# Performance work log

Measured on AMD Instinct MI355X. Metric: run time of the kernel, lower is better.

Reference implementation:

```python
import jax, jax.numpy as jnp
import numpy as np
from functools import partial

B, S, H = 4, 2048, 1152
NH, HD = 12, 96          # heads, head_dim
NM, MD = 4, 128          # memory heads (indices 6..9), mem_dim
K = 4                    # base kernel
STRIDE = 64              # NeuralMemory chunk stride
INNER = 4 * H            # GLU inner dim
CS_DIL = (1, 2, 4, 8, 16, 32)  # DilatedConvStack: config.dilations[:6]
HEAD_DIL = ((1, 2, 4), (1, 1, 1), (4, 8, 16), (8, 16, 32), (32, 64, 128),
            (64, 128, 256), (256, 512, 1024), (1, 100, 200), (1, 500, 1000),
            (1, 1024, 2048), (3, 9, 27), (5, 25, 125))
MEM_HEADS = (6, 7, 8, 9)


def setup_inputs() -> dict:
    key = jax.random.key(0)
    ks = iter(jax.random.split(key, 48))
    def nrm(shape, s=0.02):
        return jax.random.normal(next(ks), shape, jnp.float32) * s
    return {
        'x': jax.random.normal(next(ks), (B, S, H), jnp.float32),
        'norm1_w': jnp.ones((H,), jnp.float32),
        'norm2_w': jnp.ones((H,), jnp.float32),
        'norm3_w': jnp.ones((H,), jnp.float32),
        'cs_w': nrm((6, H, K), 0.1), 'cs_b': jnp.zeros((6, H), jnp.float32),
        'cs_proj_w': nrm((H, H)), 'cs_proj_b': jnp.zeros((H,), jnp.float32),
        'gate_proj_w': nrm((H, 2 * H)),
        'router_w': nrm((H, NH)), 'router_b': jnp.zeros((NH,), jnp.float32),
        'head_w': nrm((NH, 3, HD, K), 0.1), 'head_b': jnp.zeros((NH, 3, HD), jnp.float32),
        'mem_q': nrm((NM, HD, HD), 0.01), 'mem_k': nrm((NM, HD, HD), 0.01),
        'mem_v': nrm((NM, HD, MD), 0.01), 'mem_gw': nrm((NM, HD)),
        'mem_gb': jnp.full((NM,), -2.0, jnp.float32), 'mem_out': nrm((NM, MD, HD), 0.01),
        'mixgate_w': nrm((H, H)), 'mixgate_b': jnp.full((H,), 2.0, jnp.float32),
        'mixing_w': nrm((H, H)), 'mixing_b': jnp.zeros((H,), jnp.float32),
        'ffn_in_w': nrm((H, 2 * INNER)), 'ffn_out_w': nrm((INNER, H)),
        'cg_w': nrm((H,)), 'cg_b': jnp.float32(1.0),
        'sg_w': nrm((H,)), 'sg_b': jnp.float32(1.0),
        'fg_w': nrm((H,)), 'fg_b': jnp.float32(1.0),
    }


def rmsnorm(x, w, eps=1e-6):
    n = jax.lax.rsqrt(jnp.mean(x * x, axis=-1, keepdims=True) + eps)
    return x * n * w


def dconv(x, w, b, d):
    """Depthwise causal dilated conv. x:[B,S,C], w:[C,K], b:[C]."""
    s = x.shape[1]
    pad = (w.shape[1] - 1) * d
    xp = jnp.pad(x, ((0, 0), (pad, 0), (0, 0)))
    acc = b
    for j in range(w.shape[1]):
        acc = acc + w[:, j] * jax.lax.dynamic_slice_in_dim(xp, j * d, s, axis=1)
    return acc


def conv_stack(x, cs_w, cs_b, proj_w, proj_b):
    h = x
    for i, d in enumerate(CS_DIL):
        h = h + jax.nn.gelu(dconv(h, cs_w[i], cs_b[i], d), approximate=False)
    return h @ proj_w + proj_b


def neural_memory(xm, Wq, Wk, Wv, gw, gb, Wout):
    """Chunked fast-weight memory for NM heads at once. xm:[B,S,NM,HD]."""
    q = jnp.einsum('bsnd,nde->bsne', xm, Wq)
    k = jnp.einsum('bsnd,nde->bsne', xm, Wk)
    v = jnp.einsum('bsnd,ndm->bsnm', xm, Wv)
    g = jax.nn.sigmoid(jnp.einsum('bsnd,nd->bsn', xm, gw) + gb)[..., None]  # [B,S,NM,1]
    nC = S // STRIDE
    def chunk(a):  # [B,S,...] -> [nC,B,STRIDE,...]
        return a.reshape(B, nC, STRIDE, *a.shape[2:]).swapaxes(0, 1)
    q_c, kg_c, v_c = chunk(q), chunk(k * g), chunk(v)
    ga_c = chunk(g).mean(axis=2)[..., None]  # [nC,B,NM,1,1]
    M0 = jnp.zeros((B, NM, HD, MD), xm.dtype)
    def step(M, xs):
        qc, kc, vc, ga = xs
        reads = jnp.einsum('bsnd,bndm->bsnm', qc, M)
        write = jnp.einsum('bsnd,bsnm->bndm', kc, vc)
        return (1.0 - ga) * M + write, reads
    _, reads = jax.lax.scan(step, M0, (q_c, kg_c, v_c, ga_c))
    reads = reads.swapaxes(0, 1).reshape(B, S, NM, MD)
    return jnp.einsum('bsnm,nmd->bsnd', reads, Wout)


def multi_head_state(x, gate_proj_w, router_w, router_b, head_w, head_b,
                     mem_q, mem_k, mem_v, mem_gw, mem_gb, mem_out,
                     mixgate_w, mixgate_b, mixing_w, mixing_b):
    head_weights = jax.nn.sigmoid(x @ router_w + router_b)  # [B,S,NH]
    gp = x @ gate_proj_w
    xg = gp[..., :H] * jax.nn.sigmoid(gp[..., H:])
    xh = xg.reshape(B, S, NH, HD)
    outs = []
    for i in range(NH):
        h = xh[:, :, i, :]
        for j, d in enumerate(HEAD_DIL[i]):
            h = h + dconv(h, head_w[i, j], head_b[i, j], d)
        outs.append(h)
    mem = neural_memory(xh[:, :, MEM_HEADS[0]:MEM_HEADS[-1] + 1, :],
                        mem_q, mem_k, mem_v, mem_gw, mem_gb, mem_out)
    for n, i in enumerate(MEM_HEADS):
        outs[i] = outs[i] + mem[:, :, n, :]
    out = jnp.stack(outs, axis=2) * head_weights[..., None]
    out = out.reshape(B, S, H)
    out = out * jax.nn.sigmoid(out @ mixgate_w + mixgate_b)
    return out @ mixing_w + mixing_b


def glu(x, win, wout):
    h = x @ win
    return (h[..., :INNER] * jax.nn.sigmoid(h[..., INNER:])) @ wout


def reference(x, norm1_w, norm2_w, norm3_w, cs_w, cs_b, cs_proj_w, cs_proj_b,
              gate_proj_w, router_w, router_b, head_w, head_b,
              mem_q, mem_k, mem_v, mem_gw, mem_gb, mem_out,
              mixgate_w, mixgate_b, mixing_w, mixing_b,
              ffn_in_w, ffn_out_w, cg_w, cg_b, sg_w, sg_b, fg_w, fg_b):
    gc = jax.nn.sigmoid(x @ cg_w + cg_b)[..., None]
    x = x + gc * conv_stack(rmsnorm(x, norm1_w), cs_w, cs_b, cs_proj_w, cs_proj_b)
    gs = jax.nn.sigmoid(x @ sg_w + sg_b)[..., None]
    x = x + gs * multi_head_state(rmsnorm(x, norm2_w), gate_proj_w, router_w, router_b,
                                  head_w, head_b, mem_q, mem_k, mem_v, mem_gw, mem_gb,
                                  mem_out, mixgate_w, mixgate_b, mixing_w, mixing_b)
    gf = jax.nn.sigmoid(x @ fg_w + fg_b)[..., None]
    x = x + gf * glu(rmsnorm(x, norm3_w), ffn_in_w, ffn_out_w)
    return x
```

## Files before the change

### kernel.cpp

```cpp
#include <hip/hip_runtime.h>
#include <hip/hip_bf16.h>
#include <math.h>

#define TOKENS 8192
#define HDIM 1152
#define SEQ 2048
#define NHEADS 12
#define HEADD 96
#define NMEM 4
#define MEMD 128
#define FINNER 4608

typedef __hip_bfloat16 bf16;
typedef __attribute__((ext_vector_type(8))) short short8;
typedef __attribute__((ext_vector_type(4))) float floatx4;

__device__ __constant__ int g_hd_dil[NHEADS * 3] = {
    1, 2, 4,   1, 1, 1,    4, 8, 16,   8, 16, 32,
    32, 64, 128, 64, 128, 256, 256, 512, 1024, 1, 100, 200,
    1, 500, 1000, 1, 1024, 2048, 3, 9, 27, 5, 25, 125};

__device__ inline float sigm(float x) { return 1.0f / (1.0f + expf(-x)); }
__device__ inline float gelu_exact(float x) {
  return 0.5f * x * (1.0f + erff(x * 0.70710678118654752f));
}
__device__ inline float wred(float v) {
#pragma unroll
  for (int o = 32; o > 0; o >>= 1) v += __shfl_down(v, o);
  return v;
}
__device__ inline void gl_lds16(const bf16* g, bf16* l) {
  __builtin_amdgcn_global_load_lds(
      (const __attribute__((address_space(1))) unsigned int*)g,
      (__attribute__((address_space(3))) unsigned int*)l, 16, 0, 0);
}

__global__ __launch_bounds__(256) void k_transpose_bf16(
    const float* __restrict__ W, bf16* __restrict__ WT, int K, int N) {
  __shared__ float t[32][33];
  int k0 = blockIdx.y * 32, n0 = blockIdx.x * 32;
  int tx = threadIdx.x & 31, ty = threadIdx.x >> 5;
#pragma unroll
  for (int i = 0; i < 32; i += 8)
    t[ty + i][tx] = W[(size_t)(k0 + ty + i) * N + (n0 + tx)];
  __syncthreads();
#pragma unroll
  for (int i = 0; i < 32; i += 8)
    WT[(size_t)(n0 + ty + i) * K + (k0 + tx)] = __float2bfloat16(t[tx][ty + i]);
}

__global__ __launch_bounds__(256) void k_transpose_pair(
    const float* __restrict__ W, bf16* __restrict__ WT, int K, int N) {
  __shared__ float t[32][33];
  int half = N >> 1;
  int k0 = blockIdx.y * 32, n0 = blockIdx.x * 32;
  int tx = threadIdx.x & 31, ty = threadIdx.x >> 5;
  int c = (tx < 16) ? (n0 / 2 + tx) : (half + n0 / 2 + tx - 16);
#pragma unroll
  for (int i = 0; i < 32; i += 8)
    t[ty + i][tx] = W[(size_t)(k0 + ty + i) * N + c];
  __syncthreads();
#pragma unroll
  for (int i = 0; i < 32; i += 8) {
    int r = ty + i;
    int cc = (r >> 1) + (r & 1) * 16;
    WT[(size_t)(n0 + r) * K + (k0 + tx)] = __float2bfloat16(t[tx][cc]);
  }
}

__global__ __launch_bounds__(256) void k_rms_gate(
    const float* __restrict__ x, const float* __restrict__ nw,
    const float* __restrict__ gw, const float* __restrict__ gb,
    bf16* __restrict__ outb, float* outf, float* __restrict__ gout,
    int writef, const float* __restrict__ rw, const float* __restrict__ rb,
    float* __restrict__ hwout) {
  __shared__ float r1[4], r2[4];
  __shared__ float rr[4][NHEADS];
  int tok = blockIdx.x;
  int tid = threadIdx.x;
  const float* row = x + (size_t)tok * HDIM;
  float a[5];
  float s2 = 0.f, gd = 0.f;
  for (int i = tid, k = 0; i < HDIM; i += 256, ++k) {
    float v = row[i];
    a[k] = v;
    s2 += v * v;
    gd += v * gw[i];
  }
  s2 = wred(s2);
  gd = wred(gd);
  int wave = tid >> 6, lane = tid & 63;
  if (lane == 0) {
    r1[wave] = s2;
    r2[wave] = gd;
  }
  __syncthreads();
  s2 = r1[0] + r1[1] + r1[2] + r1[3];
  gd = r2[0] + r2[1] + r2[2] + r2[3];
  float rn = 1.0f / sqrtf(s2 / (float)HDIM + 1e-6f);
  if (tid == 0) gout[tok] = sigm(gd + gb[0]);
  float racc[NHEADS] = {};
  for (int i = tid, k = 0; i < HDIM; i += 256, ++k) {
    float nv = a[k] * rn * nw[i];
    outb[(size_t)tok * HDIM + i] = __float2bfloat16(nv);
    if (writef) outf[(size_t)tok * HDIM + i] = nv;
    if (hwout) {
      const float* rp = &rw[(size_t)i * NHEADS];
#pragma unroll
      for (int o = 0; o < NHEADS; ++o) racc[o] += nv * rp[o];
    }
  }
  if (hwout) {
#pragma unroll
    for (int o = 0; o < NHEADS; ++o) racc[o] = wred(racc[o]);
    if (lane == 0)
#pragma unroll
      for (int o = 0; o < NHEADS; ++o) rr[wave][o] = racc[o];
    __syncthreads();
    if (tid < NHEADS) {
      float s = rr[0][tid] + rr[1][tid] + rr[2][tid] + rr[3][tid];
      hwout[(size_t)tok * NHEADS + tid] = sigm(s + rb[tid]);
    }
  }
}

#define CS_T 256
#define CS_HALO 189
#define CS_ROWS 445
#define CS_J 28
__global__ __launch_bounds__(256) void k_convstack(
    const bf16* __restrict__ hin, bf16* __restrict__ outb,
    const float* __restrict__ cw, const float* __restrict__ cb) {
  __shared__ float cur[CS_ROWS * 16];
  int bx = blockIdx.x;
  int cs = bx % 72;
  int tile = (bx / 72) & 7;
  int b = bx / 576;
  int c0 = cs * 16;
  int S0 = tile * CS_T;
  int tid = threadIdx.x;
  int c = tid & 15, pg = tid >> 4;
  for (int i = tid; i < CS_ROWS * 8; i += 256) {
    int p = i >> 3, cc2 = (i & 7) * 2;
    int sg = S0 - CS_HALO + p;
    if (sg >= 0) {
      unsigned int u = *reinterpret_cast<const unsigned int*>(
          &hin[((size_t)(b * SEQ + sg)) * HDIM + c0 + cc2]);
      cur[p * 16 + cc2] = __uint_as_float(u << 16);
      cur[p * 16 + cc2 + 1] = __uint_as_float(u & 0xffff0000u);
    } else {
      cur[p * 16 + cc2] = 0.f;
      cur[p * 16 + cc2 + 1] = 0.f;
    }
  }
  const int dil[6] = {1, 2, 4, 8, 16, 32};
  const int Nk[6] = {3, 9, 21, 45, 93, 189};
  float nv[CS_J];
#pragma unroll
  for (int k = 0; k < 6; ++k) {
    int d = dil[k];
    float w0 = cw[((size_t)k * HDIM + c0 + c) * 4 + 0];
    float w1 = cw[((size_t)k * HDIM + c0 + c) * 4 + 1];
    float w2 = cw[((size_t)k * HDIM + c0 + c) * 4 + 2];
    float w3 = cw[((size_t)k * HDIM + c0 + c) * 4 + 3];
    float bb = cb[(size_t)k * HDIM + c0 + c];
    __syncthreads();
#pragma unroll
    for (int j = 0; j < CS_J; ++j) {
      int p = pg + 16 * j;
      if (p >= Nk[k] && p < CS_ROWS) {
        int i = p * 16 + c;
        float acc = bb + w0 * cur[i - 3 * d * 16] + w1 * cur[i - 2 * d * 16] +
                    w2 * cur[i - d * 16] + w3 * cur[i];
        int sg = S0 - CS_HALO + p;
        nv[j] = (sg >= 0) ? (cur[i] + gelu_exact(acc)) : 0.f;
      }
    }
    __syncthreads();
#pragma unroll
    for (int j = 0; j < CS_J; ++j) {
      int p = pg + 16 * j;
      if (p >= Nk[k] && p < CS_ROWS) cur[p * 16 + c] = nv[j];
    }
  }
  __syncthreads();
  for (int r = pg; r < CS_T; r += 16) {
    outb[((size_t)(b * SEQ + S0 + r)) * HDIM + c0 + c] =
        __float2bfloat16(cur[(CS_HALO + r) * 16 + c]);
  }
}

__global__ __launch_bounds__(256) void k_headconv(
    const float* __restrict__ hin, float* __restrict__ hout,
    const float* __restrict__ hw_, const float* __restrict__ hb_, int j) {
  size_t idx4 = (size_t)blockIdx.x * 256 + threadIdx.x;
  if (idx4 >= (size_t)TOKENS * HDIM / 4) return;
  size_t idx = idx4 * 4;
  int c = (int)(idx % HDIM);
  int head = c / HEADD, hd = c % HEADD;
  size_t tok = idx / HDIM;
  int s = (int)(tok % SEQ);
  int d = g_hd_dil[head * 3 + j];
  const float4* wv = reinterpret_cast<const float4*>(
      hw_ + ((size_t)(head * 3 + j) * HEADD + hd) * 4);
  float4 w0 = wv[0], w1 = wv[1], w2 = wv[2], w3 = wv[3];
  float4 bb = *reinterpret_cast<const float4*>(
      &hb_[(size_t)(head * 3 + j) * HEADD + hd]);
  float av0 = bb.x, av1 = bb.y, av2 = bb.z, av3 = bb.w;
  float4 base = *reinterpret_cast<const float4*>(&hin[idx]);
#pragma unroll
  for (int jj = 0; jj < 4; ++jj) {
    int back = (3 - jj) * d;
    if (s - back >= 0) {
      float4 t = *reinterpret_cast<const float4*>(&hin[idx - (size_t)back * HDIM]);
      float a0 = (jj == 0) ? w0.x : (jj == 1) ? w0.y : (jj == 2) ? w0.z : w0.w;
      float a1 = (jj == 0) ? w1.x : (jj == 1) ? w1.y : (jj == 2) ? w1.z : w1.w;
      float a2 = (jj == 0) ? w2.x : (jj == 1) ? w2.y : (jj == 2) ? w2.z : w2.w;
      float a3 = (jj == 0) ? w3.x : (jj == 1) ? w3.y : (jj == 2) ? w3.z : w3.w;
      av0 += a0 * t.x;
      av1 += a1 * t.y;
      av2 += a2 * t.z;
      av3 += a3 * t.w;
    }
  }
  float4 o = {base.x + av0, base.y + av1, base.z + av2, base.w + av3};
  *reinterpret_cast<float4*>(&hout[idx]) = o;
}

template <int MODE>
__global__ __launch_bounds__(256) void k_gemm(
    const bf16* __restrict__ A, const bf16* __restrict__ BT,
    const float* __restrict__ bias, const float* __restrict__ gate,
    const float* addin, float* outf, bf16* outb, int M, int N, int K) {
  __shared__ bf16 As[128 * 64];
  __shared__ bf16 Bs[128 * 64];
  const int tid = threadIdx.x;
  const int m0 = blockIdx.y * 128, n0 = blockIdx.x * 128;
  const int wave = tid >> 6, lane = tid & 63;
  const int wm = (wave & 1) * 64, wn = (wave >> 1) * 64;
  const int l16 = lane & 15, kq = lane >> 4;
  const int srow = lane >> 3;
  const int schunk = ((lane & 7) - srow) & 7;
  const bf16* gA = A + (size_t)(m0 + wave * 32 + srow) * K + schunk * 8;
  const bf16* gB = BT + (size_t)(n0 + wave * 32 + srow) * K + schunk * 8;
  bf16* lA = &As[wave * 32 * 64];
  bf16* lB = &Bs[wave * 32 * 64];
  const size_t rstride = (size_t)8 * K;
  const int col0 = ((kq + l16) & 7) * 8;
  const int col1 = ((kq + 4 + l16) & 7) * 8;
  floatx4 acc[4][4];
  floatx4 zero = {0.f, 0.f, 0.f, 0.f};
#pragma unroll
  for (int i = 0; i < 4; ++i)
#pragma unroll
    for (int jj = 0; jj < 4; ++jj) acc[i][jj] = zero;

  for (int k0 = 0; k0 < K; k0 += 64) {
    __syncthreads();
#pragma unroll
    for (int i = 0; i < 4; ++i) {
      gl_lds16(gA + k0 + i * rstride, lA + i * 8 * 64);
      gl_lds16(gB + k0 + i * rstride, lB + i * 8 * 64);
    }
    __syncthreads();
#pragma unroll
    for (int ks = 0; ks < 2; ++ks) {
      const int col = ks ? col1 : col0;
      short8 af[4], bfr[4];
#pragma unroll
      for (int t = 0; t < 4; ++t) {
        af[t] = *reinterpret_cast<const short8*>(&As[(wm + t * 16 + l16) * 64 + col]);
        bfr[t] = *reinterpret_cast<const short8*>(&Bs[(wn + t * 16 + l16) * 64 + col]);
      }
#pragma unroll
      for (int mt = 0; mt < 4; ++mt)
#pragma unroll
        for (int nt = 0; nt < 4; ++nt)
          acc[mt][nt] = __builtin_amdgcn_mfma_f32_16x16x32_bf16(
              af[mt], bfr[nt], acc[mt][nt], 0, 0, 0);
    }
  }

  if (MODE == 4 || MODE == 5) {
    const int halfN = N >> 1;
#pragma unroll
    for (int mt = 0; mt < 4; ++mt) {
#pragma unroll
      for (int nt = 0; nt < 4; ++nt) {
        int nn = n0 + wn + nt * 16 + l16;
#pragma unroll
        for (int r = 0; r < 4; ++r) {
          float v = acc[mt][nt][r];
          float g = __shfl_xor(v, 1);
          if ((lane & 1) == 0) {
            int m = m0 + wm + mt * 16 + kq * 4 + r;
            float res = v * sigm(g);
            size_t o = (size_t)m * halfN + (nn >> 1);
            if (MODE == 4) outf[o] = res;
            else outb[o] = __float2bfloat16(res);
          }
        }
      }
    }
    return;
  }

#pragma unroll
  for (int mt = 0; mt < 4; ++mt) {
#pragma unroll
    for (int nt = 0; nt < 4; ++nt) {
      int n = n0 + wn + nt * 16 + l16;
      float bv = bias ? bias[n] : 0.f;
#pragma unroll
      for (int r = 0; r < 4; ++r) {
        int m = m0 + wm + mt * 16 + kq * 4 + r;
        float v = acc[mt][nt][r] + bv;
        size_t o = (size_t)m * N + n;
        if (MODE == 2) outf[o] = addin[o] + gate[m] * v;
        else if (MODE == 6) outb[o] = __float2bfloat16(addin[o] * sigm(v));
      }
    }
  }
}

__global__ __launch_bounds__(256) void k_qkvg(
    const float* __restrict__ xh, const float* __restrict__ Wq,
    const float* __restrict__ Wk, const float* __restrict__ Wv,
    const float* __restrict__ gw, const float* __restrict__ gb,
    float* __restrict__ q, float* __restrict__ kg, float* __restrict__ v,
    float* __restrict__ gout) {
  __shared__ float xm[NMEM * HEADD];
  __shared__ float gsh[NMEM];
  int tok = blockIdx.x, tid = threadIdx.x;
  for (int i = tid; i < NMEM * HEADD; i += 256)
    xm[i] = xh[(size_t)tok * HDIM + 6 * HEADD + i];
  __syncthreads();
  if (tid < NMEM) {
    float a = gb[tid];
    for (int d = 0; d < HEADD; ++d) a += xm[tid * HEADD + d] * gw[tid * HEADD + d];
    float s = sigm(a);
    gsh[tid] = s;
    gout[tok * NMEM + tid] = s;
  }
  __syncthreads();
  for (int i = tid; i < 1280; i += 256) {
    if (i < 384) {
      int n = i / HEADD, e = i % HEADD;
      const float* W = Wq + (size_t)n * HEADD * HEADD + e;
      const float* xr = xm + n * HEADD;
      float a = 0.f;
      for (int d = 0; d < HEADD; ++d) a += xr[d] * W[(size_t)d * HEADD];
      q[(size_t)tok * 384 + i] = a;
    } else if (i < 768) {
      int i2 = i - 384;
      int n = i2 / HEADD, e = i2 % HEADD;
      const float* W = Wk + (size_t)n * HEADD * HEADD + e;
      const float* xr = xm + n * HEADD;
      float a = 0.f;
      for (int d = 0; d < HEADD; ++d) a += xr[d] * W[(size_t)d * HEADD];
      kg[(size_t)tok * 384 + i2] = a * gsh[n];
    } else {
      int i2 = i - 768;
      int n = i2 / MEMD, e = i2 % MEMD;
      const float* W = Wv + (size_t)n * HEADD * MEMD + e;
      const float* xr = xm + n * HEADD;
      float a = 0.f;
      for (int d = 0; d < HEADD; ++d) a += xr[d] * W[(size_t)d * MEMD];
      v[(size_t)tok * 512 + i2] = a;
    }
  }
}

__global__ __launch_bounds__(256) void k_memW(const float* __restrict__ kg,
                                              const float* __restrict__ v,
                                              float* __restrict__ W) {
  __shared__ float X[64 * 96];
  __shared__ float V[64 * 128];
  int bx = blockIdx.x;
  int bn = bx >> 5, ch = bx & 31;
  int b = bn >> 2, n = bn & 3;
  int t0 = b * SEQ + ch * 64;
  int tid = threadIdx.x;
  for (int i = tid; i < 64 * 96; i += 256) {
    int s = i / 96, d = i % 96;
    X[i] = kg[((size_t)(t0 + s) * NMEM + n) * HEADD + d];
  }
  for (int i = tid; i < 64 * 128; i += 256) {
    int s = i >> 7, m = i & 127;
    V[i] = v[((size_t)(t0 + s) * NMEM + n) * MEMD + m];
  }
  __syncthreads();
  float* Wb = W + (size_t)bx * 96 * 128;
  for (int t = tid; t < 768; t += 256) {
    int d0 = (t >> 5) * 4, m0 = (t & 31) * 4;
    float acc[4][4] = {};
    for (int s = 0; s < 64; ++s) {
      float4 xv = *reinterpret_cast<const float4*>(&X[s * 96 + d0]);
      float4 vv = *reinterpret_cast<const float4*>(&V[s * 128 + m0]);
      float xa[4] = {xv.x, xv.y, xv.z, xv.w};
      float va[4] = {vv.x, vv.y, vv.z, vv.w};
#pragma unroll
      for (int a = 0; a < 4; ++a)
#pragma unroll
        for (int e = 0; e < 4; ++e) acc[a][e] += xa[a] * va[e];
    }
#pragma unroll
    for (int a = 0; a < 4; ++a) {
      float4 o = {acc[a][0], acc[a][1], acc[a][2], acc[a][3]};
      *reinterpret_cast<float4*>(&Wb[(size_t)(d0 + a) * 128 + m0]) = o;
    }
  }
}

__global__ __launch_bounds__(256) void k_memscanM(const float* __restrict__ W,
                                                  const float* __restrict__ g,
                                                  float* __restrict__ Mp) {
  __shared__ float ga_sh[32];
  int bx = blockIdx.x;
  int bn = bx / 48, j = bx % 48;
  int elem = j * 256 + threadIdx.x;
  int b = bn >> 2, n = bn & 3;
  int tid = threadIdx.x;
  {
    int ch = tid >> 3, i8 = tid & 7;
    float s = 0.f;
#pragma unroll
    for (int t = 0; t < 8; ++t)
      s += g[((size_t)b * SEQ + ch * 64 + i8 * 8 + t) * NMEM + n];
#pragma unroll
    for (int o = 4; o > 0; o >>= 1) s += __shfl_down(s, o);
    if (i8 == 0) ga_sh[ch] = s * (1.0f / 64.0f);
  }
  __syncthreads();
  float wreg[32];
  size_t base0 = (size_t)bn * 32 * 12288 + elem;
#pragma unroll
  for (int ch = 0; ch < 32; ++ch) wreg[ch] = W[base0 + (size_t)ch * 12288];
  float M = 0.f;
#pragma unroll
  for (int ch = 0; ch < 32; ++ch) {
    Mp[base0 + (size_t)ch * 12288] = M;
    M = (1.f - ga_sh[ch]) * M + wreg[ch];
  }
}

__global__ __launch_bounds__(256) void k_memR(const float* __restrict__ q,
                                              const float* __restrict__ Mp,
                                              float* __restrict__ rd) {
  extern __shared__ float smem[];
  float* Q = smem;
  float* Ms = smem + 64 * 96;
  int bx = blockIdx.x;
  int bn = bx >> 5, ch = bx & 31;
  int b = bn >> 2, n = bn & 3;
  int t0 = b * SEQ + ch * 64;
  int tid = threadIdx.x;
  for (int i = tid; i < 64 * 96; i += 256) {
    int s = i / 96, d = i % 96;
    Q[i] = q[((size_t)(t0 + s) * NMEM + n) * HEADD + d];
  }
  for (int i = tid; i < 96 * 128; i += 256)
    Ms[i] = Mp[((size_t)bn * 32 + ch) * 12288 + i];
  __syncthreads();
  for (int t = tid; t < 512; t += 256) {
    int s0 = (t >> 5) * 4, m0 = (t & 31) * 4;
    float acc[4][4] = {};
    for (int k = 0; k < 96; ++k) {
      float4 mv = *reinterpret_cast<const float4*>(&Ms[k * 128 + m0]);
      float ma[4] = {mv.x, mv.y, mv.z, mv.w};
#pragma unroll
      for (int si = 0; si < 4; ++si) {
        float qs = Q[(s0 + si) * 96 + k];
#pragma unroll
        for (int mi = 0; mi < 4; ++mi) acc[si][mi] += qs * ma[mi];
      }
    }
#pragma unroll
    for (int si = 0; si < 4; ++si) {
      float4 o = {acc[si][0], acc[si][1], acc[si][2], acc[si][3]};
      *reinterpret_cast<float4*>(
          &rd[((size_t)(t0 + s0 + si) * NMEM + n) * MEMD + m0]) = o;
    }
  }
}

__global__ __launch_bounds__(256) void k_combine(
    const float* __restrict__ hconv, const float* __restrict__ reads,
    const float* __restrict__ Wout, const float* __restrict__ hw,
    float* __restrict__ outf, bf16* __restrict__ outb) {
  __shared__ float rd[NMEM * MEMD];
  int tok = blockIdx.x, tid = threadIdx.x;
  for (int i = tid; i < NMEM * MEMD; i += 256)
    rd[i] = reads[(size_t)tok * NMEM * MEMD + i];
  __syncthreads();
  for (int c = tid; c < HDIM; c += 256) {
    int head = c / HEADD, hd = c % HEADD;
    float v = hconv[(size_t)tok * HDIM + c];
    if (head >= 6 && head < 10) {
      int n = head - 6;
      const float* W = Wout + (size_t)(n * MEMD) * HEADD + hd;
      for (int m2 = 0; m2 < MEMD; ++m2) v += rd[n * MEMD + m2] * W[(size_t)m2 * HEADD];
    }
    v *= hw[tok * NHEADS + head];
    outf[(size_t)tok * HDIM + c] = v;
    outb[(size_t)tok * HDIM + c] = __float2bfloat16(v);
  }
}

extern "C" void kernel_launch(void* const* d_in, const int* in_sizes, int n_in,
                              void* d_out, int out_size, void* d_ws,
                              size_t ws_size, hipStream_t stream) {
  const float* x_in = (const float*)d_in[0];
  const float* norm1_w = (const float*)d_in[1];
  const float* norm2_w = (const float*)d_in[2];
  const float* norm3_w = (const float*)d_in[3];
  const float* cs_w = (const float*)d_in[4];
  const float* cs_b = (const float*)d_in[5];
  const float* cs_proj_w = (const float*)d_in[6];
  const float* cs_proj_b = (const float*)d_in[7];
  const float* gate_proj_w = (const float*)d_in[8];
  const float* router_w = (const float*)d_in[9];
  const float* router_b = (const float*)d_in[10];
  const float* head_w = (const float*)d_in[11];
  const float* head_b = (const float*)d_in[12];
  const float* mem_q = (const float*)d_in[13];
  const float* mem_k = (const float*)d_in[14];
  const float* mem_v = (const float*)d_in[15];
  const float* mem_gw = (const float*)d_in[16];
  const float* mem_gb = (const float*)d_in[17];
  const float* mem_out = (const float*)d_in[18];
  const float* mixgate_w = (const float*)d_in[19];
  const float* mixgate_b = (const float*)d_in[20];
  const float* mixing_w = (const float*)d_in[21];
  const float* mixing_b = (const float*)d_in[22];
  const float* ffn_in_w = (const float*)d_in[23];
  const float* ffn_out_w = (const float*)d_in[24];
  const float* cg_w = (const float*)d_in[25];
  const float* cg_b = (const float*)d_in[26];
  const float* sg_w = (const float*)d_in[27];
  const float* sg_b = (const float*)d_in[28];
  const float* fg_w = (const float*)d_in[29];
  const float* fg_b = (const float*)d_in[30];
  float* out = (float*)d_out;

  char* wsp = (char*)d_ws;
  size_t off = 0;
  auto alloc = [&](size_t bytes) -> char* {
    char* p = wsp + off;
    off += (bytes + 255) & ~(size_t)255;
    return p;
  };
  bf16* NB = (bf16*)alloc((size_t)TOKENS * HDIM * 2);
  float* F1 = (float*)alloc((size_t)TOKENS * HDIM * 4);
  float* F2 = (float*)alloc((size_t)TOKENS * HDIM * 4);
  float* F3 = (float*)alloc((size_t)TOKENS * HDIM * 4);
  char* REG = alloc((size_t)TOKENS * FINNER * 2);
  float* qb = (float*)REG;
  float* kgb = (float*)(REG + (size_t)TOKENS * 384 * 4);
  float* vb = (float*)((char*)kgb + (size_t)TOKENS * 384 * 4);
  float* rdb = (float*)((char*)vb + (size_t)TOKENS * 512 * 4);
  bf16* XG = (bf16*)REG;
  bf16* NB2 = (bf16*)REG;
  bf16* NBc = (bf16*)REG;
  bf16* WTcs = (bf16*)alloc((size_t)1152 * 1152 * 2);
  bf16* WTgp = (bf16*)alloc((size_t)2304 * 1152 * 2);
  bf16* WTmg = (bf16*)alloc((size_t)1152 * 1152 * 2);
  bf16* WTmx = (bf16*)alloc((size_t)1152 * 1152 * 2);
  float* G1 = (float*)alloc(TOKENS * 4);
  float* G2 = (float*)alloc(TOKENS * 4);
  float* G3 = (float*)alloc(TOKENS * 4);
  float* GM = (float*)alloc((size_t)TOKENS * NMEM * 4);
  float* HW = (float*)alloc((size_t)TOKENS * NHEADS * 4);
  bf16* WTfin = (bf16*)F1;
  bf16* WTfout = (bf16*)F2;
  float* Wbuf = F2;
  float* Mpref = F3;

  const int gE4 = (TOKENS * HDIM) / (4 * 256);

  k_transpose_bf16<<<dim3(36, 36), 256, 0, stream>>>(cs_proj_w, WTcs, 1152, 1152);
  k_transpose_pair<<<dim3(72, 36), 256, 0, stream>>>(gate_proj_w, WTgp, 1152, 2304);
  k_transpose_bf16<<<dim3(36, 36), 256, 0, stream>>>(mixgate_w, WTmg, 1152, 1152);
  k_transpose_bf16<<<dim3(36, 36), 256, 0, stream>>>(mixing_w, WTmx, 1152, 1152);

  k_rms_gate<<<TOKENS, 256, 0, stream>>>(x_in, norm1_w, cg_w, cg_b, NB, nullptr, G1,
                                         0, nullptr, nullptr, nullptr);
  k_convstack<<<2304, 256, 0, stream>>>(NB, NBc, cs_w, cs_b);
  k_gemm<2><<<dim3(9, 64), 256, 0, stream>>>(NBc, WTcs, cs_proj_b, G1, x_in, out,
                                             nullptr, TOKENS, 1152, 1152);

  k_rms_gate<<<TOKENS, 256, 0, stream>>>(out, norm2_w, sg_w, sg_b, NB, nullptr, G2,
                                         0, router_w, router_b, HW);
  k_gemm<4><<<dim3(18, 64), 256, 0, stream>>>(NB, WTgp, nullptr, nullptr, nullptr,
                                              F3, nullptr, TOKENS, 2304, 1152);
  k_headconv<<<gE4, 256, 0, stream>>>(F3, F1, head_w, head_b, 0);
  k_headconv<<<gE4, 256, 0, stream>>>(F1, F2, head_w, head_b, 1);
  k_headconv<<<gE4, 256, 0, stream>>>(F2, F1, head_w, head_b, 2);
  k_qkvg<<<TOKENS, 256, 0, stream>>>(F3, mem_q, mem_k, mem_v, mem_gw, mem_gb,
                                     qb, kgb, vb, GM);
  k_memW<<<512, 256, 0, stream>>>(kgb, vb, Wbuf);
  k_memscanM<<<768, 256, 0, stream>>>(Wbuf, GM, Mpref);
  k_memR<<<512, 256, (64 * 96 + 96 * 128) * 4, stream>>>(qb, Mpref, rdb);
  k_combine<<<TOKENS, 256, 0, stream>>>(F1, rdb, mem_out, HW, F2, NB);
  k_gemm<6><<<dim3(9, 64), 256, 0, stream>>>(NB, WTmg, mixgate_b, nullptr, F2,
                                             nullptr, NB2, TOKENS, 1152, 1152);
  k_gemm<2><<<dim3(9, 64), 256, 0, stream>>>(NB2, WTmx, mixing_b, G2, out, out,
                                             nullptr, TOKENS, 1152, 1152);

  k_rms_gate<<<TOKENS, 256, 0, stream>>>(out, norm3_w, fg_w, fg_b, NB, nullptr, G3,
                                         0, nullptr, nullptr, nullptr);
  k_transpose_pair<<<dim3(288, 36), 256, 0, stream>>>(ffn_in_w, WTfin, 1152, 9216);
  k_transpose_bf16<<<dim3(36, 144), 256, 0, stream>>>(ffn_out_w, WTfout, 4608, 1152);
  k_gemm<5><<<dim3(72, 64), 256, 0, stream>>>(NB, WTfin, nullptr, nullptr, nullptr,
                                              nullptr, XG, TOKENS, 9216, 1152);
  k_gemm<2><<<dim3(9, 64), 256, 0, stream>>>(XG, WTfout, nullptr, G3, out, out,
                                             nullptr, TOKENS, 1152, 4608);
}
```

Measured before the change: 1.364 ms.

## Tile memory-head QKV projection over tokens and use one wave per token in rmsnorm

k_qkvg now processes 16 tokens per block. It stages their memory-head activations transposed in shared memory and has each thread compute 4 output columns for all 16 tokens with float4 weight loads, so each weight is reused across tokens instead of re-read per token. k_rms_gate assigns one wave per token with float2 vectorised loads and stores, which removes the shared-memory cross-wave reductions and block barriers. The wider register tiles may raise register pressure. Only 1024 blocks are split across two output groups, so the second group's threads are partly idle.

Result: faster. 1.241 ms (-9.0%).

```diff
diff --git a/kernel.cpp b/kernel.cpp
--- a/kernel.cpp
+++ b/kernel.cpp
@@ -71,55 +71,52 @@
 __global__ __launch_bounds__(256) void k_rms_gate(
     const float* __restrict__ x, const float* __restrict__ nw,
     const float* __restrict__ gw, const float* __restrict__ gb,
-    bf16* __restrict__ outb, float* outf, float* __restrict__ gout,
-    int writef, const float* __restrict__ rw, const float* __restrict__ rb,
+    bf16* __restrict__ outb, float* __restrict__ gout,
+    const float* __restrict__ rw, const float* __restrict__ rb,
     float* __restrict__ hwout) {
-  __shared__ float r1[4], r2[4];
-  __shared__ float rr[4][NHEADS];
-  int tok = blockIdx.x;
-  int tid = threadIdx.x;
+  int wave = threadIdx.x >> 6, lane = threadIdx.x & 63;
+  int tok = blockIdx.x * 4 + wave;
   const float* row = x + (size_t)tok * HDIM;
-  float a[5];
+  float2 a[9];
   float s2 = 0.f, gd = 0.f;
-  for (int i = tid, k = 0; i < HDIM; i += 256, ++k) {
-    float v = row[i];
-    a[k] = v;
-    s2 += v * v;
-    gd += v * gw[i];
+#pragma unroll
+  for (int p = 0; p < 9; ++p) {
+    int i2 = lane + 64 * p;
+    a[p] = *reinterpret_cast<const float2*>(&row[i2 * 2]);
+    float2 g2 = *reinterpret_cast<const float2*>(&gw[i2 * 2]);
+    s2 += a[p].x * a[p].x + a[p].y * a[p].y;
+    gd += a[p].x * g2.x + a[p].y * g2.y;
   }
   s2 = wred(s2);
   gd = wred(gd);
-  int wave = tid >> 6, lane = tid & 63;
-  if (lane == 0) {
-    r1[wave] = s2;
-    r2[wave] = gd;
-  }
-  __syncthreads();
-  s2 = r1[0] + r1[1] + r1[2] + r1[3];
-  gd = r2[0] + r2[1] + r2[2] + r2[3];
+  if (lane == 0) gout[tok] = sigm(gd + gb[0]);
+  s2 = __shfl(s2, 0);
   float rn = 1.0f / sqrtf(s2 / (float)HDIM + 1e-6f);
-  if (tid == 0) gout[tok] = sigm(gd + gb[0]);
-  float racc[NHEADS] = {};
-  for (int i = tid, k = 0; i < HDIM; i += 256, ++k) {
-    float nv = a[k] * rn * nw[i];
-    outb[(size_t)tok * HDIM + i] = __float2bfloat16(nv);
-    if (writef) outf[(size_t)tok * HDIM + i] = nv;
+  float racc[NHEADS];
+#pragma unroll
+  for (int o = 0; o < NHEADS; ++o) racc[o] = 0.f;
+#pragma unroll
+  for (int p = 0; p < 9; ++p) {
+    int i2 = lane + 64 * p;
+    float2 w2 = *reinterpret_cast<const float2*>(&nw[i2 * 2]);
+    float nx = a[p].x * rn * w2.x;
+    float ny = a[p].y * rn * w2.y;
+    __hip_bfloat162 pr;
+    pr.x = __float2bfloat16(nx);
+    pr.y = __float2bfloat16(ny);
+    *reinterpret_cast<__hip_bfloat162*>(&outb[(size_t)tok * HDIM + i2 * 2]) = pr;
     if (hwout) {
-      const float* rp = &rw[(size_t)i * NHEADS];
-#pragma unroll
-      for (int o = 0; o < NHEADS; ++o) racc[o] += nv * rp[o];
+      const float* rp = &rw[(size_t)(i2 * 2) * NHEADS];
+#pragma unroll
+      for (int o = 0; o < NHEADS; ++o)
+        racc[o] += nx * rp[o] + ny * rp[NHEADS + o];
     }
   }
   if (hwout) {
 #pragma unroll
-    for (int o = 0; o < NHEADS; ++o) racc[o] = wred(racc[o]);
-    if (lane == 0)
-#pragma unroll
-      for (int o = 0; o < NHEADS; ++o) rr[wave][o] = racc[o];
-    __syncthreads();
-    if (tid < NHEADS) {
-      float s = rr[0][tid] + rr[1][tid] + rr[2][tid] + rr[3][tid];
-      hwout[(size_t)tok * NHEADS + tid] = sigm(s + rb[tid]);
+    for (int o = 0; o < NHEADS; ++o) {
+      float r = wred(racc[o]);
+      if (lane == 0) hwout[(size_t)tok * NHEADS + o] = sigm(r + rb[o]);
     }
   }
 }
@@ -323,50 +320,107 @@
   }
 }
 
+#define QT 16
+#define QTP 20
 __global__ __launch_bounds__(256) void k_qkvg(
     const float* __restrict__ xh, const float* __restrict__ Wq,
     const float* __restrict__ Wk, const float* __restrict__ Wv,
     const float* __restrict__ gw, const float* __restrict__ gb,
     float* __restrict__ q, float* __restrict__ kg, float* __restrict__ v,
     float* __restrict__ gout) {
-  __shared__ float xm[NMEM * HEADD];
-  __shared__ float gsh[NMEM];
-  int tok = blockIdx.x, tid = threadIdx.x;
-  for (int i = tid; i < NMEM * HEADD; i += 256)
-    xm[i] = xh[(size_t)tok * HDIM + 6 * HEADD + i];
-  __syncthreads();
-  if (tid < NMEM) {
-    float a = gb[tid];
-    for (int d = 0; d < HEADD; ++d) a += xm[tid * HEADD + d] * gw[tid * HEADD + d];
-    float s = sigm(a);
-    gsh[tid] = s;
-    gout[tok * NMEM + tid] = s;
-  }
-  __syncthreads();
-  for (int i = tid; i < 1280; i += 256) {
-    if (i < 384) {
-      int n = i / HEADD, e = i % HEADD;
-      const float* W = Wq + (size_t)n * HEADD * HEADD + e;
-      const float* xr = xm + n * HEADD;
-      float a = 0.f;
-      for (int d = 0; d < HEADD; ++d) a += xr[d] * W[(size_t)d * HEADD];
-      q[(size_t)tok * 384 + i] = a;
-    } else if (i < 768) {
-      int i2 = i - 384;
-      int n = i2 / HEADD, e = i2 % HEADD;
-      const float* W = Wk + (size_t)n * HEADD * HEADD + e;
-      const float* xr = xm + n * HEADD;
-      float a = 0.f;
-      for (int d = 0; d < HEADD; ++d) a += xr[d] * W[(size_t)d * HEADD];
-      kg[(size_t)tok * 384 + i2] = a * gsh[n];
+  __shared__ float xT[384 * QTP];
+  __shared__ float gsh[QT][NMEM];
+  int bx = blockIdx.x;
+  int grp = bx & 1;
+  int tile = bx >> 1;
+  int t0 = tile * QT;
+  int tid = threadIdx.x;
+  for (int i = tid; i < 384 * QT; i += 256) {
+    int t = i / 384, dd = i % 384;
+    xT[dd * QTP + t] = xh[(size_t)(t0 + t) * HDIM + 6 * HEADD + dd];
+  }
+  __syncthreads();
+  if (grp == 0) {
+    if (tid < 64) {
+      int t = tid >> 2, n = tid & 3;
+      float a = gb[n];
+      for (int d = 0; d < HEADD; ++d)
+        a += xT[(n * HEADD + d) * QTP + t] * gw[n * HEADD + d];
+      float s = sigm(a);
+      gsh[t][n] = s;
+      gout[(size_t)(t0 + t) * NMEM + n] = s;
+    }
+    __syncthreads();
+  }
+  int o = grp * 1024 + tid * 4;
+  if (o >= 1280) return;
+  float acc[4][QT];
+#pragma unroll
+  for (int e = 0; e < 4; ++e)
+#pragma unroll
+    for (int t = 0; t < QT; ++t) acc[e][t] = 0.f;
+
+  if (o < 768) {
+    int qk = (o >= 384) ? 1 : 0;
+    int oo = o - qk * 384;
+    int n = oo / HEADD, eb = oo % HEADD;
+    const float* W = (qk ? Wk : Wq) + (size_t)n * HEADD * HEADD;
+    const int ddb = n * HEADD;
+    for (int d = 0; d < HEADD; ++d) {
+      float4 w4 = *reinterpret_cast<const float4*>(&W[(size_t)d * HEADD + eb]);
+      const float* xr = &xT[(ddb + d) * QTP];
+#pragma unroll
+      for (int tq = 0; tq < QT / 4; ++tq) {
+        float4 xv = *reinterpret_cast<const float4*>(&xr[tq * 4]);
+        float xa[4] = {xv.x, xv.y, xv.z, xv.w};
+#pragma unroll
+        for (int u = 0; u < 4; ++u) {
+          acc[0][tq * 4 + u] += xa[u] * w4.x;
+          acc[1][tq * 4 + u] += xa[u] * w4.y;
+          acc[2][tq * 4 + u] += xa[u] * w4.z;
+          acc[3][tq * 4 + u] += xa[u] * w4.w;
+        }
+      }
+    }
+    if (qk == 0) {
+#pragma unroll
+      for (int t = 0; t < QT; ++t) {
+        float4 ov = {acc[0][t], acc[1][t], acc[2][t], acc[3][t]};
+        *reinterpret_cast<float4*>(&q[(size_t)(t0 + t) * 384 + oo]) = ov;
+      }
     } else {
-      int i2 = i - 768;
-      int n = i2 / MEMD, e = i2 % MEMD;
-      const float* W = Wv + (size_t)n * HEADD * MEMD + e;
-      const float* xr = xm + n * HEADD;
-      float a = 0.f;
-      for (int d = 0; d < HEADD; ++d) a += xr[d] * W[(size_t)d * MEMD];
-      v[(size_t)tok * 512 + i2] = a;
+#pragma unroll
+      for (int t = 0; t < QT; ++t) {
+        float g = gsh[t][n];
+        float4 ov = {acc[0][t] * g, acc[1][t] * g, acc[2][t] * g, acc[3][t] * g};
+        *reinterpret_cast<float4*>(&kg[(size_t)(t0 + t) * 384 + oo]) = ov;
+      }
+    }
+  } else {
+    int i2 = o - 768;
+    int n = i2 / MEMD, eb = i2 % MEMD;
+    const float* W = Wv + (size_t)n * HEADD * MEMD;
+    const int ddb = n * HEADD;
+    for (int d = 0; d < HEADD; ++d) {
+      float4 w4 = *reinterpret_cast<const float4*>(&W[(size_t)d * MEMD + eb]);
+      const float* xr = &xT[(ddb + d) * QTP];
+#pragma unroll
+      for (int tq = 0; tq < QT / 4; ++tq) {
+        float4 xv = *reinterpret_cast<const float4*>(&xr[tq * 4]);
+        float xa[4] = {xv.x, xv.y, xv.z, xv.w};
+#pragma unroll
+        for (int u = 0; u < 4; ++u) {
+          acc[0][tq * 4 + u] += xa[u] * w4.x;
+          acc[1][tq * 4 + u] += xa[u] * w4.y;
+          acc[2][tq * 4 + u] += xa[u] * w4.z;
+          acc[3][tq * 4 + u] += xa[u] * w4.w;
+        }
+      }
+    }
+#pragma unroll
+    for (int t = 0; t < QT; ++t) {
+      float4 ov = {acc[0][t], acc[1][t], acc[2][t], acc[3][t]};
+      *reinterpret_cast<float4*>(&v[(size_t)(t0 + t) * 512 + i2]) = ov;
     }
   }
 }
@@ -583,21 +637,21 @@
   k_transpose_bf16<<<dim3(36, 36), 256, 0, stream>>>(mixgate_w, WTmg, 1152, 1152);
   k_transpose_bf16<<<dim3(36, 36), 256, 0, stream>>>(mixing_w, WTmx, 1152, 1152);
 
-  k_rms_gate<<<TOKENS, 256, 0, stream>>>(x_in, norm1_w, cg_w, cg_b, NB, nullptr, G1,
-                                         0, nullptr, nullptr, nullptr);
+  k_rms_gate<<<2048, 256, 0, stream>>>(x_in, norm1_w, cg_w, cg_b, NB, G1,
+                                       nullptr, nullptr, nullptr);
   k_convstack<<<2304, 256, 0, stream>>>(NB, NBc, cs_w, cs_b);
   k_gemm<2><<<dim3(9, 64), 256, 0, stream>>>(NBc, WTcs, cs_proj_b, G1, x_in, out,
                                              nullptr, TOKENS, 1152, 1152);
 
-  k_rms_gate<<<TOKENS, 256, 0, stream>>>(out, norm2_w, sg_w, sg_b, NB, nullptr, G2,
-                                         0, router_w, router_b, HW);
+  k_rms_gate<<<2048, 256, 0, stream>>>(out, norm2_w, sg_w, sg_b, NB, G2,
+                                       router_w, router_b, HW);
   k_gemm<4><<<dim3(18, 64), 256, 0, stream>>>(NB, WTgp, nullptr, nullptr, nullptr,
                                               F3, nullptr, TOKENS, 2304, 1152);
   k_headconv<<<gE4, 256, 0, stream>>>(F3, F1, head_w, head_b, 0);
   k_headconv<<<gE4, 256, 0, stream>>>(F1, F2, head_w, head_b, 1);
   k_headconv<<<gE4, 256, 0, stream>>>(F2, F1, head_w, head_b, 2);
-  k_qkvg<<<TOKENS, 256, 0, stream>>>(F3, mem_q, mem_k, mem_v, mem_gw, mem_gb,
-                                     qb, kgb, vb, GM);
+  k_qkvg<<<1024, 256, 0, stream>>>(F3, mem_q, mem_k, mem_v, mem_gw, mem_gb,
+                                   qb, kgb, vb, GM);
   k_memW<<<512, 256, 0, stream>>>(kgb, vb, Wbuf);
   k_memscanM<<<768, 256, 0, stream>>>(Wbuf, GM, Mpref);
   k_memR<<<512, 256, (64 * 96 + 96 * 128) * 4, stream>>>(qb, Mpref, rdb);
@@ -607,8 +661,8 @@
   k_gemm<2><<<dim3(9, 64), 256, 0, stream>>>(NB2, WTmx, mixing_b, G2, out, out,
                                              nullptr, TOKENS, 1152, 1152);
 
-  k_rms_gate<<<TOKENS, 256, 0, stream>>>(out, norm3_w, fg_w, fg_b, NB, nullptr, G3,
-                                         0, nullptr, nullptr, nullptr);
+  k_rms_gate<<<2048, 256, 0, stream>>>(out, norm3_w, fg_w, fg_b, NB, G3,
+                                       nullptr, nullptr, nullptr);
   k_transpose_pair<<<dim3(288, 36), 256, 0, stream>>>(ffn_in_w, WTfin, 1152, 9216);
   k_transpose_bf16<<<dim3(36, 144), 256, 0, stream>>>(ffn_out_w, WTfout, 4608, 1152);
   k_gemm<5><<<dim3(72, 64), 256, 0, stream>>>(NB, WTfin, nullptr, nullptr, nullptr,
```
